# Performance work log

Measured on AMD Instinct MI355X. Metric: run time of the kernel, lower is better.

## Reference

```python
import jax, jax.numpy as jnp
import numpy as np
import math

E_LENGTH = 64


def setup_inputs() -> dict:
    key = jax.random.key(0)
    ks = jax.random.split(key, 9)
    B, L, D, N, H = 4, 1024, 1024, 16, 64
    scale = 0.05  # emulate xavier-normal scale
    return {
        "x": jax.random.normal(ks[0], (B, L, D), dtype=jnp.float32),
        "mask": jnp.ones((B, L), dtype=jnp.int32),
        "w_q": jax.random.normal(ks[1], (N, D, H), dtype=jnp.float32) * scale,
        "w_k": jax.random.normal(ks[2], (N, D, H), dtype=jnp.float32) * scale,
        "w_v": jax.random.normal(ks[3], (N, D, H), dtype=jnp.float32) * scale,
        "w_o": jax.random.normal(ks[4], (N, H, D), dtype=jnp.float32) * scale,
        "q_embed_table": jax.random.normal(ks[5], (2 * E_LENGTH - 1, H), dtype=jnp.float32) * scale,
        "k_embed_table": jax.random.normal(ks[6], (2 * E_LENGTH - 1, H), dtype=jnp.float32) * scale,
        "v_embed_table": jax.random.normal(ks[7], (2 * E_LENGTH - 1, H), dtype=jnp.float32) * scale,
    }


def reference(x, mask, w_q, w_k, w_v, w_o, q_embed_table, k_embed_table, v_embed_table):
    # x: [B, L, d_model], mask: [B, L]
    L = x.shape[1]
    d_qkv = w_q.shape[-1]
    e = E_LENGTH

    q = jnp.einsum('blm,nmh->bnlh', x, w_q)
    k = jnp.einsum('blm,nmh->bnlh', x, w_k)
    v = jnp.einsum('blm,nmh->bnlh', x, w_v)

    pos = jnp.arange(L)
    # clipped relative distance indices in [0, 2e-2]
    dist = jnp.clip(pos[:, None] - pos[None, :], -(e - 1), e - 1) + (e - 1)  # [L, L]

    scores = jnp.einsum('bnid,bnjd->bnij', q, k)
    # mode contains 'q': key-side bias uses k_embedding
    k_embed = k_embed_table[dist]  # [L, L, d]
    scores = scores + jnp.einsum('bnjd,ijd->bnij', k, k_embed)
    # mode contains 'k': query-side bias uses q_embedding
    q_embed = q_embed_table[dist]  # [L, L, d]
    scores = scores + jnp.einsum('bnid,ijd->bnij', q, q_embed)

    scores = scores / math.sqrt(d_qkv)
    scores = jnp.where((mask == 0)[:, None, None, :], jnp.float32(-1e9), scores)
    p_attn = jax.nn.softmax(scores, axis=-1)  # [B, N, L, L]

    out = jnp.einsum('bnij,bnjd->bnid', p_attn, v)
    # mode contains 'v': value-side relative bias
    v_embed = v_embed_table[dist]  # [L, L, d]
    out = out + jnp.einsum('bnij,ijd->bnid', p_attn, v_embed)

    # per-head output projection, then sum over heads
    return jnp.einsum('bnid,ndm->bim', out, w_o)
```

## Files before the change

### kernel.cpp

```cpp
#include <hip/hip_runtime.h>


typedef __bf16 bf16x8 __attribute__((ext_vector_type(8)));
typedef float f32x4 __attribute__((ext_vector_type(4)));
typedef unsigned int u32x4 __attribute__((ext_vector_type(4)));

__device__ __forceinline__ unsigned short f2bf(float f) {
    unsigned int u = __builtin_bit_cast(unsigned int, f);
    u += 0x7fffu + ((u >> 16) & 1u);
    return (unsigned short)(u >> 16);
}
__device__ __forceinline__ float bf2f(unsigned short s) {
    unsigned int u = ((unsigned int)s) << 16;
    return __builtin_bit_cast(float, u);
}

__device__ __forceinline__ void gl2lds16(const unsigned short* g, unsigned short* l) {
    __builtin_amdgcn_global_load_lds(
        (const __attribute__((address_space(1))) unsigned int*)g,
        (__attribute__((address_space(3))) unsigned int*)l, 16, 0, 0);
}

__global__ void convert_kernel(const float* __restrict__ x,
                               const float* __restrict__ wq,
                               const float* __restrict__ wk,
                               const float* __restrict__ wv,
                               const float* __restrict__ wo,
                               const float* __restrict__ qe,
                               const float* __restrict__ ke,
                               const float* __restrict__ ve,
                               unsigned short* __restrict__ x_bf,
                               unsigned short* __restrict__ wqkv_bt,
                               unsigned short* __restrict__ wo_bt,
                               unsigned short* __restrict__ qe_bf,
                               unsigned short* __restrict__ ke_bf,
                               unsigned short* __restrict__ ve_t)
{
    const size_t R0 = 4u * 1024 * 1024;
    const size_t R1 = R0 + 3u * 1024 * 1024;
    const size_t R2 = R1 + 1024u * 1024;
    const size_t R3 = R2 + 8192;
    const size_t R4 = R3 + 8192;
    const size_t R5 = R4 + 8192;
    size_t stride = (size_t)gridDim.x * blockDim.x;
    for (size_t i = (size_t)blockIdx.x * blockDim.x + threadIdx.x; i < R5; i += stride) {
        if (i < R0) {
            x_bf[i] = f2bf(x[i]);
        } else if (i < R1) {
            size_t j = i - R0;
            int which = (int)(j >> 20);
            int rem = (int)(j & 0xFFFFF);
            int n = rem >> 16, d = (rem >> 6) & 1023, h = rem & 63;
            const float* w = which == 0 ? wq : which == 1 ? wk : wv;
            wqkv_bt[(size_t)(which * 1024 + n * 64 + h) * 1024 + d] = f2bf(w[rem]);
        } else if (i < R2) {
            int rem = (int)(i - R1);
            int n = rem >> 16, h = (rem >> 10) & 63, m = rem & 1023;
            wo_bt[(size_t)m * 1024 + n * 64 + h] = f2bf(wo[rem]);
        } else if (i < R3) {
            int idx = (int)(i - R2);
            int e = idx >> 6;
            qe_bf[idx] = (e < 127) ? f2bf(qe[idx]) : 0;
        } else if (i < R4) {
            int idx = (int)(i - R3);
            int e = idx >> 6;
            ke_bf[idx] = (e < 127) ? f2bf(ke[idx]) : 0;
        } else {
            int idx = (int)(i - R4);
            int h = idx >> 7, e = idx & 127;
            ve_t[idx] = (e < 127) ? f2bf(ve[e * 64 + h]) : 0;
        }
    }
}

template<int MODE>
__global__ __launch_bounds__(256) void gemm_bt_kernel(
    const unsigned short* __restrict__ A,
    const unsigned short* __restrict__ Bt,
    int K, int lda, int ldb,
    void* __restrict__ C0, void* __restrict__ C1, void* __restrict__ C2,
    int ldc)
{
    __shared__ unsigned short As[128 * 64];
    __shared__ unsigned short Bs[128 * 64];
    const int m0 = blockIdx.y * 128;
    const int n0 = blockIdx.x * 128;
    const int tid = threadIdx.x;
    const int lane = tid & 63;
    const int w = tid >> 6;
    const int wr = w >> 1, wc = w & 1;
    const int g = lane >> 4, c16 = lane & 15;

    f32x4 acc[4][4];
#pragma unroll
    for (int i = 0; i < 4; ++i)
#pragma unroll
        for (int j = 0; j < 4; ++j) acc[i][j] = f32x4{0.f, 0.f, 0.f, 0.f};

    for (int kt = 0; kt < K; kt += 64) {
#pragma unroll
        for (int c = 0; c < 4; ++c) {
            int chunk = c * 256 + tid;
            int row = chunk >> 3, col = (chunk & 7) * 8;
            unsigned short* ldsA = &As[(c * 256 + w * 64) * 8];
            unsigned short* ldsB = &Bs[(c * 256 + w * 64) * 8];
            gl2lds16(A  + (size_t)(m0 + row) * lda + kt + col, ldsA);
            gl2lds16(Bt + (size_t)(n0 + row) * ldb + kt + col, ldsB);
        }
        __syncthreads();
#pragma unroll
        for (int ks = 0; ks < 2; ++ks) {
            bf16x8 af[4], bfr[4];
#pragma unroll
            for (int mi = 0; mi < 4; ++mi)
                af[mi] = __builtin_bit_cast(bf16x8,
                    *reinterpret_cast<const u32x4*>(&As[(wr * 64 + mi * 16 + c16) * 64 + ks * 32 + g * 8]));
#pragma unroll
            for (int ni = 0; ni < 4; ++ni)
                bfr[ni] = __builtin_bit_cast(bf16x8,
                    *reinterpret_cast<const u32x4*>(&Bs[(wc * 64 + ni * 16 + c16) * 64 + ks * 32 + g * 8]));
#pragma unroll
            for (int mi = 0; mi < 4; ++mi)
#pragma unroll
                for (int ni = 0; ni < 4; ++ni)
                    acc[mi][ni] = __builtin_amdgcn_mfma_f32_16x16x32_bf16(af[mi], bfr[ni], acc[mi][ni], 0, 0, 0);
        }
        __syncthreads();
    }

#pragma unroll
    for (int mi = 0; mi < 4; ++mi) {
#pragma unroll
        for (int ni = 0; ni < 4; ++ni) {
#pragma unroll
            for (int r = 0; r < 4; ++r) {
                int m = m0 + wr * 64 + mi * 16 + g * 4 + r;
                int c = n0 + wc * 64 + ni * 16 + c16;
                float v = acc[mi][ni][r];
                if (MODE == 0) {
                    int b = m >> 10, l = m & 1023;
                    int which = c >> 10, n = (c >> 6) & 15, h = c & 63;
                    if (which == 2) {
                        ((unsigned short*)C2)[(((size_t)b * 16 + n) * 64 + h) * 1024 + l] = f2bf(v);
                    } else {
                        unsigned short* dst = (unsigned short*)(which == 0 ? C0 : C1);
                        dst[(((size_t)b * 16 + n) * 1024 + l) * 64 + h] = f2bf(v);
                    }
                } else if (MODE == 1) {
                    ((unsigned short*)C0)[(size_t)m * ldc + c] = f2bf(v);
                    if (C1 && (c == 0 || c == 126))
                        ((unsigned short*)C1)[(size_t)(c ? 65536 : 0) + m] = f2bf(v);
                } else {
                    ((float*)C0)[(size_t)m * ldc + c] = v;
                }
            }
        }
    }
}

#define ATTN_LDS_BYTES 54784

__global__ __launch_bounds__(512, 4) void attn_kernel(
    const unsigned short* __restrict__ q_buf,
    const unsigned short* __restrict__ k_buf,
    const unsigned short* __restrict__ v_t,
    const unsigned short* __restrict__ q_proj,
    const unsigned short* __restrict__ k_proj,
    const unsigned short* __restrict__ kp_edge,
    const unsigned short* __restrict__ ve_t,
    const int* __restrict__ mask,
    unsigned short* __restrict__ attn_out)
{
    extern __shared__ char smem[];
    unsigned short* Ks = (unsigned short*)smem;
    unsigned short* Vt = (unsigned short*)(smem + 9216);
    unsigned short* Ps = (unsigned short*)(smem + 18432);
    unsigned short* kp = (unsigned short*)(smem + 36864);
    float* mj   = (float*)(smem + 54272);
    float* kpej = (float*)(smem + 54528);
    unsigned short* veT = (unsigned short*)smem;
    unsigned short* peB = (unsigned short*)(smem + 17408);
    float* lrow = (float*)(smem + 52224);

    const int id = blockIdx.x;
    const int bn = id & 63;
    const int ib = id >> 6;
    const int b = bn >> 4;
    const int i0 = ib * 128;
    const int tid = threadIdx.x;
    const int lane = tid & 63;
    const int w = tid >> 6;
    const int g = lane >> 4, c16 = lane & 15;
    const int il = tid >> 2;
    const int part = tid & 3;

    const int sr = tid >> 3, sc = (tid & 7) * 8;

    bf16x8 qf[2];
    {
        const unsigned short* qrow = q_buf + ((size_t)bn * 1024 + i0 + w * 16 + c16) * 64;
        qf[0] = __builtin_bit_cast(bf16x8, *reinterpret_cast<const u32x4*>(qrow + g * 8));
        qf[1] = __builtin_bit_cast(bf16x8, *reinterpret_cast<const u32x4*>(qrow + 32 + g * 8));
    }
    f32x4 qp0v, qp126v;
#pragma unroll
    for (int r = 0; r < 4; ++r) {
        size_t row = (size_t)bn * 1024 + i0 + w * 16 + g * 4 + r;
        qp0v[r]   = 0.125f * bf2f(q_proj[row * 128 + 0]);
        qp126v[r] = 0.125f * bf2f(q_proj[row * 128 + 126]);
    }

    float peR[32];
#pragma unroll
    for (int k = 0; k < 32; ++k) peR[k] = 0.f;
    float lreg = 0.f, acc0 = 0.f, acc126 = 0.f;
    f32x4 accO[4];
#pragma unroll
    for (int i = 0; i < 4; ++i) accO[i] = f32x4{0.f, 0.f, 0.f, 0.f};

    const int jlo = 2 * ib - 1, jhi = 2 * ib + 2;

    for (int jt = 0; jt < 16; ++jt) {
        const int j0 = jt * 64;
        const bool need_kp = (jt >= jlo) && (jt <= jhi);

        {
            u32x4 kv = *reinterpret_cast<const u32x4*>(k_buf + ((size_t)bn * 1024 + j0 + sr) * 64 + sc);
            u32x4 vv = *reinterpret_cast<const u32x4*>(v_t + ((size_t)bn * 64 + sr) * 1024 + j0 + sc);
            *reinterpret_cast<u32x4*>(&Ks[sr * 72 + sc]) = kv;
            *reinterpret_cast<u32x4*>(&Vt[sr * 72 + sc]) = vv;
        }
        if (need_kp) {
#pragma unroll
            for (int c = 0; c < 2; ++c) {
                int chunk = tid + c * 512;
                int row = chunk >> 4, col = (chunk & 15) * 8;
                u32x4 v = *reinterpret_cast<const u32x4*>(k_proj + ((size_t)bn * 1024 + j0 + row) * 128 + col);
                *reinterpret_cast<u32x4*>(&kp[row * 136 + col]) = v;
            }
        }
        if (tid < 64) {
            mj[tid] = mask[b * 1024 + j0 + tid] ? 1.f : 0.f;
            kpej[tid] = 0.125f * bf2f(kp_edge[(size_t)(jt < 2 * ib ? 65536 : 0) + bn * 1024 + j0 + tid]);
        }
        __syncthreads();

        f32x4 sacc[4];
#pragma unroll
        for (int nf = 0; nf < 4; ++nf) sacc[nf] = f32x4{0.f, 0.f, 0.f, 0.f};
#pragma unroll
        for (int ks = 0; ks < 2; ++ks)
#pragma unroll
            for (int nf = 0; nf < 4; ++nf) {
                bf16x8 kf = __builtin_bit_cast(bf16x8,
                    *reinterpret_cast<const u32x4*>(&Ks[(nf * 16 + c16) * 72 + ks * 32 + g * 8]));
                sacc[nf] = __builtin_amdgcn_mfma_f32_16x16x32_bf16(qf[ks], kf, sacc[nf], 0, 0, 0);
            }

        const int dw = i0 + w * 16 - j0;
        if (dw < 126 && dw > -78) {
            const int d0 = i0 - j0 + 63;
            const unsigned short* qpg = q_proj + ((size_t)bn * 1024 + i0) * 128;
#pragma unroll
            for (int nf = 0; nf < 4; ++nf) {
                int j_l = nf * 16 + c16;
                float mfl = mj[j_l];
#pragma unroll
                for (int r = 0; r < 4; ++r) {
                    int i_l = w * 16 + g * 4 + r;
                    int e = d0 + i_l - j_l;
                    e = e < 0 ? 0 : (e > 126 ? 126 : e);
                    float s = sacc[nf][r] + bf2f(kp[j_l * 136 + e]) + bf2f(qpg[i_l * 128 + e]);
                    s *= 0.125f;
                    float p = (mfl > 0.f) ? __expf(s) : 0.f;
                    Ps[i_l * 72 + j_l] = f2bf(p);
                }
            }
        } else {
            const f32x4 qpc = (dw >= 126) ? qp126v : qp0v;
#pragma unroll
            for (int nf = 0; nf < 4; ++nf) {
                int j_l = nf * 16 + c16;
                float kv = kpej[j_l];
                float mfl = mj[j_l];
#pragma unroll
                for (int r = 0; r < 4; ++r) {
                    float s = sacc[nf][r] * 0.125f + kv + qpc[r];
                    float p = (mfl > 0.f) ? __expf(s) : 0.f;
                    Ps[(w * 16 + g * 4 + r) * 72 + j_l] = f2bf(p);
                }
            }
        }

#pragma unroll
        for (int ks = 0; ks < 2; ++ks) {
            bf16x8 pf = __builtin_bit_cast(bf16x8,
                *reinterpret_cast<const u32x4*>(&Ps[(w * 16 + c16) * 72 + ks * 32 + g * 8]));
#pragma unroll
            for (int nf2 = 0; nf2 < 4; ++nf2) {
                bf16x8 vf = __builtin_bit_cast(bf16x8,
                    *reinterpret_cast<const u32x4*>(&Vt[(nf2 * 16 + c16) * 72 + ks * 32 + g * 8]));
                accO[nf2] = __builtin_amdgcn_mfma_f32_16x16x32_bf16(pf, vf, accO[nf2], 0, 0, 0);
            }
        }

        {
            bf16x8 s0 = __builtin_bit_cast(bf16x8,
                *reinterpret_cast<const u32x4*>(&Ps[il * 72 + part * 16]));
            bf16x8 s1 = __builtin_bit_cast(bf16x8,
                *reinterpret_cast<const u32x4*>(&Ps[il * 72 + part * 16 + 8]));
            float v[16];
#pragma unroll
            for (int m = 0; m < 8; ++m) { v[m] = (float)s0[m]; v[8 + m] = (float)s1[m]; }
            float rs = 0.f;
#pragma unroll
            for (int m = 0; m < 16; ++m) rs += v[m];
            rs += __shfl_xor(rs, 1);
            rs += __shfl_xor(rs, 2);
            lreg += rs;

            const int base = i0 + il - j0 + 63;
            if (base >= 189) {
                acc126 += rs;
            } else if (base <= 0) {
                acc0 += rs;
            } else {
                float b0 = 0.f, b126 = 0.f;
#pragma unroll
                for (int m = 0; m < 16; ++m) {
                    int jl = part * 16 + m;
                    if (jl >= base) b0 += v[m];
                    if (jl <= base - 126) b126 += v[m];
                }
                b0 += __shfl_xor(b0, 1);     b0 += __shfl_xor(b0, 2);
                b126 += __shfl_xor(b126, 1); b126 += __shfl_xor(b126, 2);
                if (part == 0) peR[0] += b0;
                if (part == 3) peR[30] += b126;
#pragma unroll
                for (int k = 0; k < 32; ++k) {
                    int e = part * 32 + k;
                    int jl = base - e;
                    if (e >= 1 && e <= 125 && jl >= 0 && jl < 64)
                        peR[k] += bf2f(Ps[il * 72 + jl]);
                }
            }
        }
        __syncthreads();
    }

    if (part == 0) peR[0] += acc0;
    if (part == 3) peR[30] += acc126;

#pragma unroll
    for (int c = 0; c < 2; ++c) {
        int chunk = tid + c * 512;
        int h = chunk >> 4, col = (chunk & 15) * 8;
        u32x4 vv = *reinterpret_cast<const u32x4*>(ve_t + h * 128 + col);
        *reinterpret_cast<u32x4*>(&veT[h * 136 + col]) = vv;
    }
#pragma unroll
    for (int kk = 0; kk < 4; ++kk) {
        bf16x8 pk;
#pragma unroll
        for (int e2 = 0; e2 < 8; ++e2) pk[e2] = (__bf16)peR[kk * 8 + e2];
        *reinterpret_cast<u32x4*>(&peB[il * 136 + part * 32 + kk * 8]) =
            __builtin_bit_cast(u32x4, pk);
    }
    if (part == 0) lrow[il] = lreg;
    __syncthreads();

#pragma unroll
    for (int ks = 0; ks < 4; ++ks) {
        bf16x8 pf = __builtin_bit_cast(bf16x8,
            *reinterpret_cast<const u32x4*>(&peB[(w * 16 + c16) * 136 + ks * 32 + g * 8]));
#pragma unroll
        for (int nf2 = 0; nf2 < 4; ++nf2) {
            bf16x8 vf = __builtin_bit_cast(bf16x8,
                *reinterpret_cast<const u32x4*>(&veT[(nf2 * 16 + c16) * 136 + ks * 32 + g * 8]));
            accO[nf2] = __builtin_amdgcn_mfma_f32_16x16x32_bf16(pf, vf, accO[nf2], 0, 0, 0);
        }
    }

#pragma unroll
    for (int nf2 = 0; nf2 < 4; ++nf2) {
#pragma unroll
        for (int r = 0; r < 4; ++r) {
            int i_l = w * 16 + g * 4 + r;
            int h = nf2 * 16 + c16;
            float vv = accO[nf2][r] / lrow[i_l];
            attn_out[(((size_t)b * 1024 + i0 + i_l) * 16 + (bn & 15)) * 64 + h] = f2bf(vv);
        }
    }
}

extern "C" void kernel_launch(void* const* d_in, const int* in_sizes, int n_in,
                              void* d_out, int out_size, void* d_ws, size_t ws_size,
                              hipStream_t stream)
{
    const float* x  = (const float*)d_in[0];
    const int* mask = (const int*)d_in[1];
    const float* wq = (const float*)d_in[2];
    const float* wk = (const float*)d_in[3];
    const float* wv = (const float*)d_in[4];
    const float* wo = (const float*)d_in[5];
    const float* qe = (const float*)d_in[6];
    const float* ke = (const float*)d_in[7];
    const float* ve = (const float*)d_in[8];

    char* ws = (char*)d_ws;
    size_t off = 0;
    auto carve = [&](size_t bytes) -> char* {
        char* p = ws + off;
        off += (bytes + 255) & ~(size_t)255;
        return p;
    };
    unsigned short* x_bf    = (unsigned short*)carve(4096ull * 1024 * 2);
    unsigned short* wqkv_bt = (unsigned short*)carve(3072ull * 1024 * 2);
    unsigned short* wo_bt   = (unsigned short*)carve(1024ull * 1024 * 2);
    unsigned short* qe_bf   = (unsigned short*)carve(128ull * 64 * 2);
    unsigned short* ke_bf   = (unsigned short*)carve(128ull * 64 * 2);
    unsigned short* ve_t    = (unsigned short*)carve(64ull * 128 * 2);
    unsigned short* q_buf   = (unsigned short*)carve(65536ull * 64 * 2);
    unsigned short* k_buf   = (unsigned short*)carve(65536ull * 64 * 2);
    unsigned short* v_t     = (unsigned short*)carve(65536ull * 64 * 2);
    unsigned short* q_proj  = (unsigned short*)carve(65536ull * 128 * 2);
    unsigned short* k_proj  = (unsigned short*)carve(65536ull * 128 * 2);
    unsigned short* kp_edge = (unsigned short*)carve(2ull * 65536 * 2);
    unsigned short* attn_o  = (unsigned short*)carve(4096ull * 1024 * 2);
    (void)ws_size; (void)in_sizes; (void)n_in; (void)out_size;

    convert_kernel<<<2048, 256, 0, stream>>>(x, wq, wk, wv, wo, qe, ke, ve,
                                             x_bf, wqkv_bt, wo_bt, qe_bf, ke_bf, ve_t);

    gemm_bt_kernel<0><<<dim3(24, 32), 256, 0, stream>>>(
        x_bf, wqkv_bt, 1024, 1024, 1024, q_buf, k_buf, v_t, 0);

    gemm_bt_kernel<1><<<dim3(1, 512), 256, 0, stream>>>(
        q_buf, qe_bf, 64, 64, 64, q_proj, nullptr, nullptr, 128);
    gemm_bt_kernel<1><<<dim3(1, 512), 256, 0, stream>>>(
        k_buf, ke_bf, 64, 64, 64, k_proj, kp_edge, nullptr, 128);

    hipFuncSetAttribute((const void*)attn_kernel,
                        hipFuncAttributeMaxDynamicSharedMemorySize, ATTN_LDS_BYTES);
    attn_kernel<<<512, 512, ATTN_LDS_BYTES, stream>>>(
        q_buf, k_buf, v_t, q_proj, k_proj, kp_edge, ve_t, mask, attn_o);

    gemm_bt_kernel<2><<<dim3(8, 32), 256, 0, stream>>>(
        attn_o, wo_bt, 1024, 1024, 1024, d_out, nullptr, nullptr, 1024);
}
```

Baseline: 227.3 us.

## Double-buffer K/V tiles in attention with register prefetch and MFMA priority

The attention loop now issues global loads for the next K/V/k_proj/mask tile into registers before computing on the current tile, then writes them into an alternate LDS buffer at the end of the iteration. This hides global-load latency behind the MFMA and softmax work. s_setprio raises wave priority around the MFMA sections. The attention output buffer reuses the x_bf workspace. The cost is more LDS (73728 bytes) and more registers, which may lower occupancy, plus an extra barrier when k_proj is reloaded.

```diff
diff --git a/kernel.cpp b/kernel.cpp
--- a/kernel.cpp
+++ b/kernel.cpp
@@ -158,7 +158,7 @@
     }
 }
 
-#define ATTN_LDS_BYTES 54784
+#define ATTN_LDS_BYTES 73728
 
 __global__ __launch_bounds__(512, 4) void attn_kernel(
     const unsigned short* __restrict__ q_buf,
@@ -172,12 +172,10 @@
     unsigned short* __restrict__ attn_out)
 {
     extern __shared__ char smem[];
-    unsigned short* Ks = (unsigned short*)smem;
-    unsigned short* Vt = (unsigned short*)(smem + 9216);
-    unsigned short* Ps = (unsigned short*)(smem + 18432);
-    unsigned short* kp = (unsigned short*)(smem + 36864);
-    float* mj   = (float*)(smem + 54272);
-    float* kpej = (float*)(smem + 54528);
+    unsigned short* Ps = (unsigned short*)(smem + 36864);
+    unsigned short* kp = (unsigned short*)(smem + 55296);
+    float* mj2   = (float*)(smem + 72704);
+    float* kpej2 = (float*)(smem + 73216);
     unsigned short* veT = (unsigned short*)smem;
     unsigned short* peB = (unsigned short*)(smem + 17408);
     float* lrow = (float*)(smem + 52224);
@@ -194,7 +192,44 @@
     const int il = tid >> 2;
     const int part = tid & 3;
 
-    const int sr = tid >> 3, sc = (tid & 7) * 8;
+    const int jlo = 2 * ib - 1, jhi = 2 * ib + 2;
+
+    const int sr = tid >> 3,  sc = (tid & 7) * 8;
+    const int kpr = tid >> 4, kpc = (tid & 15) * 8;
+
+    u32x4 kreg, vreg, kpreg0, kpreg1;
+    int mjr = 0; unsigned short kper = 0;
+
+    auto issue_loads = [&](int jt, bool wantkp) {
+        const int j0 = jt * 64;
+        kreg = *reinterpret_cast<const u32x4*>(k_buf + ((size_t)bn * 1024 + j0 + sr) * 64 + sc);
+        vreg = *reinterpret_cast<const u32x4*>(v_t + ((size_t)bn * 64 + sr) * 1024 + j0 + sc);
+        if (wantkp) {
+            kpreg0 = *reinterpret_cast<const u32x4*>(k_proj + ((size_t)bn * 1024 + j0 + kpr) * 128 + kpc);
+            kpreg1 = *reinterpret_cast<const u32x4*>(k_proj + ((size_t)bn * 1024 + j0 + 32 + kpr) * 128 + kpc);
+        }
+        if (tid < 64) {
+            mjr = mask[b * 1024 + j0 + tid];
+            kper = kp_edge[(size_t)(jt < 2 * ib ? 65536 : 0) + bn * 1024 + j0 + tid];
+        }
+    };
+    auto write_tile = [&](int bufp, bool wantkp) {
+        unsigned short* Ksw = (unsigned short*)(smem + bufp * 9216);
+        unsigned short* Vtw = (unsigned short*)(smem + 18432 + bufp * 9216);
+        *reinterpret_cast<u32x4*>(&Ksw[sr * 72 + sc]) = kreg;
+        *reinterpret_cast<u32x4*>(&Vtw[sr * 72 + sc]) = vreg;
+        if (wantkp) {
+            *reinterpret_cast<u32x4*>(&kp[kpr * 136 + kpc]) = kpreg0;
+            *reinterpret_cast<u32x4*>(&kp[(32 + kpr) * 136 + kpc]) = kpreg1;
+        }
+        if (tid < 64) {
+            mj2[bufp * 64 + tid] = mjr ? 1.f : 0.f;
+            kpej2[bufp * 64 + tid] = 0.125f * bf2f(kper);
+        }
+    };
+
+    const bool kp0 = (0 >= jlo && 0 <= jhi);
+    issue_loads(0, kp0);
 
     bf16x8 qf[2];
     {
@@ -210,6 +245,9 @@
         qp126v[r] = 0.125f * bf2f(q_proj[row * 128 + 126]);
     }
 
+    write_tile(0, kp0);
+    __syncthreads();
+
     float peR[32];
 #pragma unroll
     for (int k = 0; k < 32; ++k) peR[k] = 0.f;
@@ -218,36 +256,24 @@
 #pragma unroll
     for (int i = 0; i < 4; ++i) accO[i] = f32x4{0.f, 0.f, 0.f, 0.f};
 
-    const int jlo = 2 * ib - 1, jhi = 2 * ib + 2;
-
     for (int jt = 0; jt < 16; ++jt) {
+        const int cur = jt & 1;
         const int j0 = jt * 64;
-        const bool need_kp = (jt >= jlo) && (jt <= jhi);
-
-        {
-            u32x4 kv = *reinterpret_cast<const u32x4*>(k_buf + ((size_t)bn * 1024 + j0 + sr) * 64 + sc);
-            u32x4 vv = *reinterpret_cast<const u32x4*>(v_t + ((size_t)bn * 64 + sr) * 1024 + j0 + sc);
-            *reinterpret_cast<u32x4*>(&Ks[sr * 72 + sc]) = kv;
-            *reinterpret_cast<u32x4*>(&Vt[sr * 72 + sc]) = vv;
-        }
-        if (need_kp) {
-#pragma unroll
-            for (int c = 0; c < 2; ++c) {
-                int chunk = tid + c * 512;
-                int row = chunk >> 4, col = (chunk & 15) * 8;
-                u32x4 v = *reinterpret_cast<const u32x4*>(k_proj + ((size_t)bn * 1024 + j0 + row) * 128 + col);
-                *reinterpret_cast<u32x4*>(&kp[row * 136 + col]) = v;
-            }
-        }
-        if (tid < 64) {
-            mj[tid] = mask[b * 1024 + j0 + tid] ? 1.f : 0.f;
-            kpej[tid] = 0.125f * bf2f(kp_edge[(size_t)(jt < 2 * ib ? 65536 : 0) + bn * 1024 + j0 + tid]);
-        }
-        __syncthreads();
+        const unsigned short* Ks = (const unsigned short*)(smem + cur * 9216);
+        const unsigned short* Vt = (const unsigned short*)(smem + 18432 + cur * 9216);
+        const float* mj = &mj2[cur * 64];
+        const float* kpej = &kpej2[cur * 64];
+
+        bool nextkp = false;
+        if (jt < 15) {
+            nextkp = (jt + 1 >= jlo) && (jt + 1 <= jhi);
+            issue_loads(jt + 1, nextkp);
+        }
 
         f32x4 sacc[4];
 #pragma unroll
         for (int nf = 0; nf < 4; ++nf) sacc[nf] = f32x4{0.f, 0.f, 0.f, 0.f};
+        __builtin_amdgcn_s_setprio(1);
 #pragma unroll
         for (int ks = 0; ks < 2; ++ks)
 #pragma unroll
@@ -256,6 +282,7 @@
                     *reinterpret_cast<const u32x4*>(&Ks[(nf * 16 + c16) * 72 + ks * 32 + g * 8]));
                 sacc[nf] = __builtin_amdgcn_mfma_f32_16x16x32_bf16(qf[ks], kf, sacc[nf], 0, 0, 0);
             }
+        __builtin_amdgcn_s_setprio(0);
 
         const int dw = i0 + w * 16 - j0;
         if (dw < 126 && dw > -78) {
@@ -292,6 +319,7 @@
             }
         }
 
+        __builtin_amdgcn_s_setprio(1);
 #pragma unroll
         for (int ks = 0; ks < 2; ++ks) {
             bf16x8 pf = __builtin_bit_cast(bf16x8,
@@ -303,6 +331,7 @@
                 accO[nf2] = __builtin_amdgcn_mfma_f32_16x16x32_bf16(pf, vf, accO[nf2], 0, 0, 0);
             }
         }
+        __builtin_amdgcn_s_setprio(0);
 
         {
             bf16x8 s0 = __builtin_bit_cast(bf16x8,
@@ -345,7 +374,14 @@
                 }
             }
         }
-        __syncthreads();
+
+        if (jt < 15) {
+            if (nextkp) __syncthreads();
+            write_tile(cur ^ 1, nextkp);
+            __syncthreads();
+        } else {
+            __syncthreads();
+        }
     }
 
     if (part == 0) peR[0] += acc0;
@@ -426,7 +462,7 @@
     unsigned short* q_proj  = (unsigned short*)carve(65536ull * 128 * 2);
     unsigned short* k_proj  = (unsigned short*)carve(65536ull * 128 * 2);
     unsigned short* kp_edge = (unsigned short*)carve(2ull * 65536 * 2);
-    unsigned short* attn_o  = (unsigned short*)carve(4096ull * 1024 * 2);
+    unsigned short* attn_o  = x_bf;
     (void)ws_size; (void)in_sizes; (void)n_in; (void)out_size;
 
     convert_kernel<<<2048, 256, 0, stream>>>(x, wq, wk, wv, wo, qe, ke, ve,
```

After: 253.3 us. 11.4% more time.

## Merge Q/K embedding projections into one launch and use narrower output GEMM tiles

Applied to the files above, without the earlier changes.

The two separate projection GEMM launches (q·qe and k·ke) are merged into one specialised proj_kernel with a single-K-step load and no loop. The final output projection switches from 128x128 tiles (256 blocks) to a dedicated 128x64-tile kernel with 512 blocks, to fill more CUs on the GPU. The attention output buffer now reuses the x_bf workspace instead of a separate allocation. The narrower tiles re-read the A matrix more often, and the new GEMM loop has no double buffering.

```diff
diff --git a/kernel.cpp b/kernel.cpp
--- a/kernel.cpp
+++ b/kernel.cpp
@@ -146,16 +146,153 @@
                         unsigned short* dst = (unsigned short*)(which == 0 ? C0 : C1);
                         dst[(((size_t)b * 16 + n) * 1024 + l) * 64 + h] = f2bf(v);
                     }
-                } else if (MODE == 1) {
-                    ((unsigned short*)C0)[(size_t)m * ldc + c] = f2bf(v);
-                    if (C1 && (c == 0 || c == 126))
-                        ((unsigned short*)C1)[(size_t)(c ? 65536 : 0) + m] = f2bf(v);
-                } else {
-                    ((float*)C0)[(size_t)m * ldc + c] = v;
                 }
             }
         }
     }
+}
+
+__global__ __launch_bounds__(256) void proj_kernel(
+    const unsigned short* __restrict__ q_buf,
+    const unsigned short* __restrict__ k_buf,
+    const unsigned short* __restrict__ qe_bf,
+    const unsigned short* __restrict__ ke_bf,
+    unsigned short* __restrict__ q_proj,
+    unsigned short* __restrict__ k_proj,
+    unsigned short* __restrict__ kp_edge)
+{
+    __shared__ unsigned short As[128 * 64];
+    __shared__ unsigned short Bs[128 * 64];
+    const int by = blockIdx.y;
+    const int which = by >> 9;
+    const int m0 = (by & 511) * 128;
+    const unsigned short* A  = which ? k_buf : q_buf;
+    const unsigned short* Bt = which ? ke_bf : qe_bf;
+    unsigned short* C0 = which ? k_proj : q_proj;
+
+    const int tid = threadIdx.x;
+    const int lane = tid & 63;
+    const int w = tid >> 6;
+    const int wr = w >> 1, wc = w & 1;
+    const int g = lane >> 4, c16 = lane & 15;
+
+    f32x4 acc[4][4];
+#pragma unroll
+    for (int i = 0; i < 4; ++i)
+#pragma unroll
+        for (int j = 0; j < 4; ++j) acc[i][j] = f32x4{0.f, 0.f, 0.f, 0.f};
+
+#pragma unroll
+    for (int c = 0; c < 4; ++c) {
+        int chunk = c * 256 + tid;
+        int row = chunk >> 3, col = (chunk & 7) * 8;
+        unsigned short* ldsA = &As[(c * 256 + w * 64) * 8];
+        unsigned short* ldsB = &Bs[(c * 256 + w * 64) * 8];
+        gl2lds16(A  + (size_t)(m0 + row) * 64 + col, ldsA);
+        gl2lds16(Bt + (size_t)row * 64 + col, ldsB);
+    }
+    __syncthreads();
+#pragma unroll
+    for (int ks = 0; ks < 2; ++ks) {
+        bf16x8 af[4], bfr[4];
+#pragma unroll
+        for (int mi = 0; mi < 4; ++mi)
+            af[mi] = __builtin_bit_cast(bf16x8,
+                *reinterpret_cast<const u32x4*>(&As[(wr * 64 + mi * 16 + c16) * 64 + ks * 32 + g * 8]));
+#pragma unroll
+        for (int ni = 0; ni < 4; ++ni)
+            bfr[ni] = __builtin_bit_cast(bf16x8,
+                *reinterpret_cast<const u32x4*>(&Bs[(wc * 64 + ni * 16 + c16) * 64 + ks * 32 + g * 8]));
+#pragma unroll
+        for (int mi = 0; mi < 4; ++mi)
+#pragma unroll
+            for (int ni = 0; ni < 4; ++ni)
+                acc[mi][ni] = __builtin_amdgcn_mfma_f32_16x16x32_bf16(af[mi], bfr[ni], acc[mi][ni], 0, 0, 0);
+    }
+
+#pragma unroll
+    for (int mi = 0; mi < 4; ++mi) {
+#pragma unroll
+        for (int ni = 0; ni < 4; ++ni) {
+#pragma unroll
+            for (int r = 0; r < 4; ++r) {
+                int m = m0 + wr * 64 + mi * 16 + g * 4 + r;
+                int c = wc * 64 + ni * 16 + c16;
+                float v = acc[mi][ni][r];
+                C0[(size_t)m * 128 + c] = f2bf(v);
+                if (which && (c == 0 || c == 126))
+                    kp_edge[(size_t)(c ? 65536 : 0) + m] = f2bf(v);
+            }
+        }
+    }
+}
+
+__global__ __launch_bounds__(256) void gemm_n64_kernel(
+    const unsigned short* __restrict__ A,
+    const unsigned short* __restrict__ Bt,
+    float* __restrict__ C)
+{
+    __shared__ unsigned short As[128 * 64];
+    __shared__ unsigned short Bs[64 * 64];
+    const int m0 = blockIdx.y * 128;
+    const int n0 = blockIdx.x * 64;
+    const int tid = threadIdx.x;
+    const int lane = tid & 63;
+    const int w = tid >> 6;
+    const int g = lane >> 4, c16 = lane & 15;
+
+    f32x4 acc[2][4];
+#pragma unroll
+    for (int i = 0; i < 2; ++i)
+#pragma unroll
+        for (int j = 0; j < 4; ++j) acc[i][j] = f32x4{0.f, 0.f, 0.f, 0.f};
+
+    for (int kt = 0; kt < 1024; kt += 64) {
+#pragma unroll
+        for (int c = 0; c < 4; ++c) {
+            int chunk = c * 256 + tid;
+            int row = chunk >> 3, col = (chunk & 7) * 8;
+            unsigned short* ldsA = &As[(c * 256 + w * 64) * 8];
+            gl2lds16(A + (size_t)(m0 + row) * 1024 + kt + col, ldsA);
+        }
+#pragma unroll
+        for (int c = 0; c < 2; ++c) {
+            int chunk = c * 256 + tid;
+            int row = chunk >> 3, col = (chunk & 7) * 8;
+            unsigned short* ldsB = &Bs[(c * 256 + w * 64) * 8];
+            gl2lds16(Bt + (size_t)(n0 + row) * 1024 + kt + col, ldsB);
+        }
+        __syncthreads();
+#pragma unroll
+        for (int ks = 0; ks < 2; ++ks) {
+            bf16x8 af[2], bfr[4];
+#pragma unroll
+            for (int mi = 0; mi < 2; ++mi)
+                af[mi] = __builtin_bit_cast(bf16x8,
+                    *reinterpret_cast<const u32x4*>(&As[(w * 32 + mi * 16 + c16) * 64 + ks * 32 + g * 8]));
+#pragma unroll
+            for (int ni = 0; ni < 4; ++ni)
+                bfr[ni] = __builtin_bit_cast(bf16x8,
+                    *reinterpret_cast<const u32x4*>(&Bs[(ni * 16 + c16) * 64 + ks * 32 + g * 8]));
+#pragma unroll
+            for (int mi = 0; mi < 2; ++mi)
+#pragma unroll
+                for (int ni = 0; ni < 4; ++ni)
+                    acc[mi][ni] = __builtin_amdgcn_mfma_f32_16x16x32_bf16(af[mi], bfr[ni], acc[mi][ni], 0, 0, 0);
+        }
+        __syncthreads();
+    }
+
+#pragma unroll
+    for (int mi = 0; mi < 2; ++mi)
+#pragma unroll
+        for (int ni = 0; ni < 4; ++ni)
+#pragma unroll
+            for (int r = 0; r < 4; ++r) {
+                int m = m0 + w * 32 + mi * 16 + g * 4 + r;
+                int cc = n0 + ni * 16 + c16;
+                C[(size_t)m * 1024 + cc] = acc[mi][ni][r];
+            }
 }
 
 #define ATTN_LDS_BYTES 54784
@@ -194,7 +331,9 @@
     const int il = tid >> 2;
     const int part = tid & 3;
 
-    const int sr = tid >> 3, sc = (tid & 7) * 8;
+    const int jlo = 2 * ib - 1, jhi = 2 * ib + 2;
+
+    const int sr = tid >> 3,  sc = (tid & 7) * 8;
 
     bf16x8 qf[2];
     {
@@ -217,8 +356,6 @@
     f32x4 accO[4];
 #pragma unroll
     for (int i = 0; i < 4; ++i) accO[i] = f32x4{0.f, 0.f, 0.f, 0.f};
-
-    const int jlo = 2 * ib - 1, jhi = 2 * ib + 2;
 
     for (int jt = 0; jt < 16; ++jt) {
         const int j0 = jt * 64;
@@ -426,7 +563,7 @@
     unsigned short* q_proj  = (unsigned short*)carve(65536ull * 128 * 2);
     unsigned short* k_proj  = (unsigned short*)carve(65536ull * 128 * 2);
     unsigned short* kp_edge = (unsigned short*)carve(2ull * 65536 * 2);
-    unsigned short* attn_o  = (unsigned short*)carve(4096ull * 1024 * 2);
+    unsigned short* attn_o  = x_bf;
     (void)ws_size; (void)in_sizes; (void)n_in; (void)out_size;
 
     convert_kernel<<<2048, 256, 0, stream>>>(x, wq, wk, wv, wo, qe, ke, ve,
@@ -435,16 +572,13 @@
     gemm_bt_kernel<0><<<dim3(24, 32), 256, 0, stream>>>(
         x_bf, wqkv_bt, 1024, 1024, 1024, q_buf, k_buf, v_t, 0);
 
-    gemm_bt_kernel<1><<<dim3(1, 512), 256, 0, stream>>>(
-        q_buf, qe_bf, 64, 64, 64, q_proj, nullptr, nullptr, 128);
-    gemm_bt_kernel<1><<<dim3(1, 512), 256, 0, stream>>>(
-        k_buf, ke_bf, 64, 64, 64, k_proj, kp_edge, nullptr, 128);
+    proj_kernel<<<dim3(1, 1024), 256, 0, stream>>>(
+        q_buf, k_buf, qe_bf, ke_bf, q_proj, k_proj, kp_edge);
 
     hipFuncSetAttribute((const void*)attn_kernel,
                         hipFuncAttributeMaxDynamicSharedMemorySize, ATTN_LDS_BYTES);
     attn_kernel<<<512, 512, ATTN_LDS_BYTES, stream>>>(
         q_buf, k_buf, v_t, q_proj, k_proj, kp_edge, ve_t, mask, attn_o);
 
-    gemm_bt_kernel<2><<<dim3(8, 32), 256, 0, stream>>>(
-        attn_o, wo_bt, 1024, 1024, 1024, d_out, nullptr, nullptr, 1024);
-}
+    gemm_n64_kernel<<<dim3(16, 32), 256, 0, stream>>>(attn_o, wo_bt, (float*)d_out);
+}
```

Result: faster. 218.5 us (-3.9%).
